# Optimization experiments

Measured on AMD Instinct MI355X. Metric: run time of the kernel, lower is better.

Reference implementation:

```python
import jax, jax.numpy as jnp
import numpy as np

C = 256
C8 = C // 8
B, H, W = 8, 64, 64


def setup_inputs() -> dict:
    key = jax.random.key(0)
    ks = jax.random.split(key, 8)
    scale = 1.0 / np.sqrt(C)
    return {
        "x": jax.random.normal(ks[0], (B, C, H, W), dtype=jnp.float32),
        "wq": jax.random.normal(ks[1], (C8, C), dtype=jnp.float32) * scale,
        "bq": jax.random.normal(ks[2], (C8,), dtype=jnp.float32) * 0.01,
        "wk": jax.random.normal(ks[3], (C8, C), dtype=jnp.float32) * scale,
        "bk": jax.random.normal(ks[4], (C8,), dtype=jnp.float32) * 0.01,
        "wv": jax.random.normal(ks[5], (C, C), dtype=jnp.float32) * scale,
        "bv": jax.random.normal(ks[6], (C,), dtype=jnp.float32) * 0.01,
        "gamma": jax.random.normal(ks[7], (1,), dtype=jnp.float32) * 0.1,
    }


def reference(x, wq, bq, wk, bk, wv, bv, gamma):
    b, c, h, w = x.shape
    n = h * w
    xf = x.reshape(b, c, n)  # flatten spatial; 1x1 conv == channel matmul
    q = jnp.einsum('oc,bcn->bno', wq, xf) + bq            # [b, n, c/8]
    k = jnp.einsum('oc,bcn->bon', wk, xf) + bk[:, None]   # [b, c/8, n]
    v = jnp.einsum('oc,bcn->bon', wv, xf) + bv[:, None]   # [b, c, n]
    attn = jax.nn.softmax(jnp.einsum('bno,bom->bnm', q, k), axis=2)  # [b,n,n]
    out = jnp.einsum('bcm,bnm->bcn', v, attn).reshape(b, c, h, w)
    return x + gamma[0] * out
```

## Files before the change

### kernel.cpp

```cpp
#include <hip/hip_runtime.h>

typedef unsigned short ushort_t;
typedef __bf16 bf16x8 __attribute__((ext_vector_type(8)));
typedef float f32x16 __attribute__((ext_vector_type(16)));
typedef float f32x4v __attribute__((ext_vector_type(4)));
typedef unsigned int u32x4 __attribute__((ext_vector_type(4)));
typedef unsigned int u32x2 __attribute__((ext_vector_type(2)));

#define L2E 1.44269504088896340736f

__device__ __forceinline__ unsigned cvt_pk_bf16(float a, float b) {
  unsigned r;
  asm("v_cvt_pk_bf16_f32 %0, %1, %2" : "=v"(r) : "v"(a), "v"(b));
  return r;
}

__device__ __forceinline__ float fast_exp2(float v) {
#if __has_builtin(__builtin_amdgcn_exp2f)
  return __builtin_amdgcn_exp2f(v);
#else
  return exp2f(v);
#endif
}

__device__ __forceinline__ f32x16 mfma32(u32x4 a, u32x4 b, f32x16 c) {
  return __builtin_amdgcn_mfma_f32_32x32x16_bf16(
      __builtin_bit_cast(bf16x8, a), __builtin_bit_cast(bf16x8, b), c, 0, 0, 0);
}

__global__ __launch_bounds__(512, 2) void proj_kernel(
    const float* __restrict__ x,
    const float* __restrict__ wq, const float* __restrict__ bq,
    const float* __restrict__ wk, const float* __restrict__ bk,
    const float* __restrict__ wv, const float* __restrict__ bv,
    ushort_t* __restrict__ qtg, ushort_t* __restrict__ ktg,
    ushort_t* __restrict__ vtg)
{
  __shared__ ushort_t xT[64 * 256];

  const int tid  = threadIdx.x;
  const int b    = blockIdx.x & 7;
  const int nt   = blockIdx.x >> 3;
  const int n0   = nt * 64;
  const int lane = tid & 63;
  const int wid  = tid >> 6;
  const int l31  = lane & 31;
  const int half = lane >> 5;

  {
    const int xn = tid & 63;
    const int cg = tid >> 6;
    const int ng = xn >> 5, l = xn & 31;
    const float* xb = x + (size_t)b * 256 * 4096 + n0 + xn;
    #pragma unroll
    for (int s = 0; s < 4; ++s) {
      const int c0 = cg * 32 + s * 8;
      float f0 = xb[(size_t)(c0+0)*4096], f1 = xb[(size_t)(c0+1)*4096];
      float f2 = xb[(size_t)(c0+2)*4096], f3 = xb[(size_t)(c0+3)*4096];
      float f4 = xb[(size_t)(c0+4)*4096], f5 = xb[(size_t)(c0+5)*4096];
      float f6 = xb[(size_t)(c0+6)*4096], f7 = xb[(size_t)(c0+7)*4096];
      u32x4 pk;
      pk.x = cvt_pk_bf16(f0, f1); pk.y = cvt_pk_bf16(f2, f3);
      pk.z = cvt_pk_bf16(f4, f5); pk.w = cvt_pk_bf16(f6, f7);
      const int c8 = c0 >> 3;
      *(u32x4*)(xT + ((c8 * 2 + ng) * 32 + l) * 8) = pk;
    }
  }
  __syncthreads();

  const int og = wid & 1, ng = (wid >> 1) & 1, rr = wid >> 2;
  const int n  = n0 + ng * 32 + l31;

  for (int ot = rr; ot < 5; ot += 2) {
    const int o0 = og * 160 + ot * 32;
    const int grow = o0 + l31;
    const float* wrow = (o0 < 32) ? (wq + grow * 256)
                      : (o0 < 64) ? (wk + (grow - 32) * 256)
                                  : (wv + (grow - 64) * 256);
    f32x16 acc = {};
    #pragma unroll
    for (int kc = 0; kc < 16; ++kc) {
      f32x4v g0 = *(const f32x4v*)(wrow + kc * 16 + half * 8);
      f32x4v g1 = *(const f32x4v*)(wrow + kc * 16 + half * 8 + 4);
      u32x4 af;
      af.x = cvt_pk_bf16(g0.x, g0.y); af.y = cvt_pk_bf16(g0.z, g0.w);
      af.z = cvt_pk_bf16(g1.x, g1.y); af.w = cvt_pk_bf16(g1.z, g1.w);
      u32x4 bf = *(const u32x4*)(xT + ((kc * 2 + half) * 2 + ng) * 256 + l31 * 8);
      acc = mfma32(af, bf, acc);
    }
    if (o0 < 64) {
      ushort_t* dst = (o0 == 0) ? qtg : ktg;
      const float* bias = (o0 == 0) ? bq : bk;
      const size_t rowbase = ((size_t)b * 4096 + n) * 32;
      #pragma unroll
      for (int g = 0; g < 4; ++g) {
        const int ob = 8 * g + 4 * half;
        float v0 = acc[4*g+0] + bias[ob+0];
        float v1 = acc[4*g+1] + bias[ob+1];
        float v2 = acc[4*g+2] + bias[ob+2];
        float v3 = acc[4*g+3] + bias[ob+3];
        u32x2 pk2; pk2.x = cvt_pk_bf16(v0, v1); pk2.y = cvt_pk_bf16(v2, v3);
        *(u32x2*)(dst + rowbase + ob) = pk2;
      }
    } else {
      const int cbase = o0 - 64;
      #pragma unroll
      for (int r = 0; r < 16; ++r) {
        const int c = cbase + (r & 3) + 8 * (r >> 2) + 4 * half;
        float v = acc[r] + bv[c];
        vtg[((size_t)b * 256 + c) * 4096 + n] = (ushort_t)cvt_pk_bf16(v, v);
      }
    }
  }
}

#define SOFTMAX_PACK(S, MR, LR, OB, PB0, PB1) do {                            \
  float y0 = fmaxf(fmaxf(S[0],  S[1]),  fmaxf(S[2],  S[3]));                  \
  float y1 = fmaxf(fmaxf(S[4],  S[5]),  fmaxf(S[6],  S[7]));                  \
  float y2 = fmaxf(fmaxf(S[8],  S[9]),  fmaxf(S[10], S[11]));                 \
  float y3 = fmaxf(fmaxf(S[12], S[13]), fmaxf(S[14], S[15]));                 \
  const float vmx  = fmaxf(fmaxf(y0, y1), fmaxf(y2, y3));                     \
  const float pmax = fmaxf(vmx, __shfl_xor(vmx, 32, 64));                     \
  if (__any(pmax > (MR) + 8.0f)) {                                            \
    const float mnew = fmaxf((MR), pmax);                                     \
    const float sc   = fast_exp2(((MR) - mnew) * L2E);                        \
    (LR) *= sc;                                                               \
    _Pragma("unroll")                                                         \
    for (int ct_ = 0; ct_ < 4; ++ct_) {                                       \
      _Pragma("unroll")                                                       \
      for (int r_ = 0; r_ < 16; ++r_) oacc[(OB) + ct_][r_] *= sc;             \
    }                                                                         \
    (MR) = mnew;                                                              \
  }                                                                           \
  const float ml2 = (MR) * L2E;                                               \
  float p_[16];                                                               \
  _Pragma("unroll")                                                           \
  for (int r_ = 0; r_ < 16; ++r_) p_[r_] = fast_exp2(fmaf(S[r_], L2E, -ml2)); \
  const float ps = (((p_[0]+p_[1])+(p_[2]+p_[3])) + ((p_[4]+p_[5])+(p_[6]+p_[7]))) \
                 + (((p_[8]+p_[9])+(p_[10]+p_[11])) + ((p_[12]+p_[13])+(p_[14]+p_[15]))); \
  (LR) += ps + __shfl_xor(ps, 32, 64);                                        \
  const unsigned wd0 = cvt_pk_bf16(p_[0],  p_[1]),  wd1 = cvt_pk_bf16(p_[2],  p_[3]);  \
  const unsigned wd2 = cvt_pk_bf16(p_[4],  p_[5]),  wd3 = cvt_pk_bf16(p_[6],  p_[7]);  \
  const unsigned wd4 = cvt_pk_bf16(p_[8],  p_[9]),  wd5 = cvt_pk_bf16(p_[10], p_[11]); \
  const unsigned wd6 = cvt_pk_bf16(p_[12], p_[13]), wd7 = cvt_pk_bf16(p_[14], p_[15]); \
  const unsigned pw0 = __shfl_xor((int)wd0, 32, 64), pw1 = __shfl_xor((int)wd1, 32, 64); \
  const unsigned pw2 = __shfl_xor((int)wd2, 32, 64), pw3 = __shfl_xor((int)wd3, 32, 64); \
  const unsigned pw4 = __shfl_xor((int)wd4, 32, 64), pw5 = __shfl_xor((int)wd5, 32, 64); \
  const unsigned pw6 = __shfl_xor((int)wd6, 32, 64), pw7 = __shfl_xor((int)wd7, 32, 64); \
  PB0.x = half ? pw2 : wd0;  PB0.y = half ? pw3 : wd1;                        \
  PB0.z = half ? wd2 : pw0;  PB0.w = half ? wd3 : pw1;                        \
  PB1.x = half ? pw6 : wd4;  PB1.y = half ? pw7 : wd5;                        \
  PB1.z = half ? wd6 : pw4;  PB1.w = half ? wd7 : pw5;                        \
} while (0)

__global__ __launch_bounds__(256, 2) void attn_kernel(
    const ushort_t* __restrict__ qtg, const ushort_t* __restrict__ ktg,
    const ushort_t* __restrict__ vtg, const float* __restrict__ x,
    const float* __restrict__ gamma, float* __restrict__ out)
{
  __shared__ float obuf[16][16][64];
  __shared__ float mls[2][8][64];

  const int tid  = threadIdx.x;
  const int lane = tid & 63;
  const int wid  = tid >> 6;
  const int l31  = lane & 31;
  const int half = lane >> 5;
  const int ks   = wid & 1;
  const int cs   = wid >> 1;
  const int b    = blockIdx.x & 7;
  const int qt   = blockIdx.x >> 3;
  const int qbase = qt * 64;

  const ushort_t* ktb = ktg + (size_t)b * 4096 * 32;
  const ushort_t* vr  = vtg + ((size_t)b * 256 + cs * 128 + l31) * 4096;

  const ushort_t* qr0 = qtg + ((size_t)b * 4096 + qbase + l31) * 32;
  const ushort_t* qr1 = qr0 + 32 * 32;
  const u32x4 qf00 = *(const u32x4*)(qr0 + half * 8);
  const u32x4 qf01 = *(const u32x4*)(qr0 + 16 + half * 8);
  const u32x4 qf10 = *(const u32x4*)(qr1 + half * 8);
  const u32x4 qf11 = *(const u32x4*)(qr1 + 16 + half * 8);

  u32x4 kf0 = *(const u32x4*)(ktb + (size_t)(ks * 32 + l31) * 32 + half * 8);
  u32x4 kf1 = *(const u32x4*)(ktb + (size_t)(ks * 32 + l31) * 32 + 16 + half * 8);
  u32x4 kn0 = kf0, kn1 = kf1;

  float mr0 = -3.0e38f, mr1 = -3.0e38f, lr0 = 0.0f, lr1 = 0.0f;
  f32x16 oacc[8] = {};

  for (int i = 0; i < 64; ++i) {
    const int t = 2 * i + ks;

    u32x4 vf[4][2];
    #pragma unroll
    for (int ct = 0; ct < 4; ++ct)
      #pragma unroll
      for (int mh = 0; mh < 2; ++mh)
        vf[ct][mh] = *(const u32x4*)(vr + (size_t)ct * 32 * 4096 +
                                     t * 32 + mh * 16 + half * 8);

    f32x16 s0 = {}, s1 = {};
    __builtin_amdgcn_s_setprio(1);
    s0 = mfma32(kf0, qf00, s0);  s0 = mfma32(kf1, qf01, s0);
    s1 = mfma32(kf0, qf10, s1);  s1 = mfma32(kf1, qf11, s1);
    __builtin_amdgcn_s_setprio(0);

    if (i < 63) {
      const ushort_t* kr = ktb + (size_t)((t + 2) * 32 + l31) * 32;
      kn0 = *(const u32x4*)(kr + half * 8);
      kn1 = *(const u32x4*)(kr + 16 + half * 8);
    }

    {
      u32x4 pb0, pb1;
      SOFTMAX_PACK(s0, mr0, lr0, 0, pb0, pb1);
      __builtin_amdgcn_s_setprio(1);
      #pragma unroll
      for (int ct = 0; ct < 4; ++ct) {
        oacc[ct] = mfma32(vf[ct][0], pb0, oacc[ct]);
        oacc[ct] = mfma32(vf[ct][1], pb1, oacc[ct]);
      }
      __builtin_amdgcn_s_setprio(0);
    }
    {
      u32x4 pb0, pb1;
      SOFTMAX_PACK(s1, mr1, lr1, 4, pb0, pb1);
      __builtin_amdgcn_s_setprio(1);
      #pragma unroll
      for (int ct = 0; ct < 4; ++ct) {
        oacc[4 + ct] = mfma32(vf[ct][0], pb0, oacc[4 + ct]);
        oacc[4 + ct] = mfma32(vf[ct][1], pb1, oacc[4 + ct]);
      }
      __builtin_amdgcn_s_setprio(0);
    }

    kf0 = kn0; kf1 = kn1;
  }

  mls[0][wid * 2 + 0][lane] = mr0;  mls[0][wid * 2 + 1][lane] = mr1;
  mls[1][wid * 2 + 0][lane] = lr0;  mls[1][wid * 2 + 1][lane] = lr1;
  __syncthreads();
  const int pw = (wid ^ 1) * 2;
  const float mO0 = mls[0][pw + 0][lane], lO0 = mls[1][pw + 0][lane];
  const float mO1 = mls[0][pw + 1][lane], lO1 = mls[1][pw + 1][lane];
  const float mS0 = fmaxf(mr0, mO0), mS1 = fmaxf(mr1, mO1);
  const float aS0 = fast_exp2((mr0 - mS0) * L2E), aO0 = fast_exp2((mO0 - mS0) * L2E);
  const float aS1 = fast_exp2((mr1 - mS1) * L2E), aO1 = fast_exp2((mO1 - mS1) * L2E);
  const float li0 = 1.0f / (aS0 * lr0 + aO0 * lO0);
  const float li1 = 1.0f / (aS1 * lr1 + aO1 * lO1);

  if (ks == 1) {
    #pragma unroll
    for (int qt2 = 0; qt2 < 2; ++qt2) {
      const float aS = qt2 ? aS1 : aS0;
      #pragma unroll
      for (int ct = 0; ct < 4; ++ct) {
        const int slot = cs * 8 + qt2 * 4 + ct;
        #pragma unroll
        for (int r = 0; r < 16; ++r)
          obuf[slot][r][lane] = aS * oacc[qt2 * 4 + ct][r];
      }
    }
  }
  __syncthreads();
  if (ks == 0) {
    const float g = gamma[0];
    const size_t base = (size_t)b * 256 * 4096;
    #pragma unroll
    for (int qt2 = 0; qt2 < 2; ++qt2) {
      const float aS = qt2 ? aS1 : aS0;
      const float li = qt2 ? li1 : li0;
      const size_t n = qbase + qt2 * 32 + l31;
      #pragma unroll
      for (int ct = 0; ct < 4; ++ct) {
        const int slot = cs * 8 + qt2 * 4 + ct;
        #pragma unroll
        for (int r = 0; r < 16; ++r) {
          const float oS = aS * oacc[qt2 * 4 + ct][r] + obuf[slot][r][lane];
          const int c = cs * 128 + ct * 32 + (r & 3) + 8 * (r >> 2) + 4 * half;
          const size_t off = base + (size_t)c * 4096 + n;
          out[off] = x[off] + g * (oS * li);
        }
      }
    }
  }
}

extern "C" void kernel_launch(void* const* d_in, const int* in_sizes, int n_in,
                              void* d_out, int out_size, void* d_ws, size_t ws_size,
                              hipStream_t stream) {
  (void)in_sizes; (void)n_in; (void)out_size; (void)ws_size;
  const float* x     = (const float*)d_in[0];
  const float* wq    = (const float*)d_in[1];
  const float* bq    = (const float*)d_in[2];
  const float* wk    = (const float*)d_in[3];
  const float* bk    = (const float*)d_in[4];
  const float* wv    = (const float*)d_in[5];
  const float* bv    = (const float*)d_in[6];
  const float* gamma = (const float*)d_in[7];
  float* out = (float*)d_out;

  ushort_t* ws  = (ushort_t*)d_ws;
  ushort_t* qtw = ws;
  ushort_t* ktw = ws + (size_t)8*4096*32;
  ushort_t* vww = ws + (size_t)2*8*4096*32;

  proj_kernel<<<512, 512, 0, stream>>>(x, wq, bq, wk, bk, wv, bv, qtw, ktw, vww);
  attn_kernel<<<512, 256, 0, stream>>>(qtw, ktw, vww, x, gamma, out);
}
```

Baseline: 285.4 us.

## Stage V tiles through LDS with async double buffering and stage projection weights

In the attention kernel, V tiles are no longer loaded from global memory straight into registers. Each wave now issues global_load_lds copies into a per-wave double-buffered LDS region one iteration ahead, synchronised with an explicit vmcnt wait, so the load latency can overlap with compute. The LDS is shared through a union with the output reduction buffer. The projection kernel also converts weights to bf16 into a swizzled LDS tile cooperatively and lets each wave compute two output tiles, which removes redundant per-wave global weight loads. The cost is more LDS use, which may lower occupancy, and hand-tuned waitcnt counts that are fragile.

```diff
diff --git a/kernel.cpp b/kernel.cpp
--- a/kernel.cpp
+++ b/kernel.cpp
@@ -37,6 +37,7 @@
     ushort_t* __restrict__ vtg)
 {
   __shared__ ushort_t xT[64 * 256];
+  __shared__ ushort_t wl[160 * 128];
 
   const int tid  = threadIdx.x;
   const int b    = blockIdx.x & 7;
@@ -63,52 +64,81 @@
       pk.x = cvt_pk_bf16(f0, f1); pk.y = cvt_pk_bf16(f2, f3);
       pk.z = cvt_pk_bf16(f4, f5); pk.w = cvt_pk_bf16(f6, f7);
       const int c8 = c0 >> 3;
-      *(u32x4*)(xT + ((c8 * 2 + ng) * 32 + l) * 8) = pk;
-    }
-  }
-  __syncthreads();
-
-  const int og = wid & 1, ng = (wid >> 1) & 1, rr = wid >> 2;
-  const int n  = n0 + ng * 32 + l31;
-
-  for (int ot = rr; ot < 5; ot += 2) {
-    const int o0 = og * 160 + ot * 32;
-    const int grow = o0 + l31;
-    const float* wrow = (o0 < 32) ? (wq + grow * 256)
-                      : (o0 < 64) ? (wk + (grow - 32) * 256)
-                                  : (wv + (grow - 64) * 256);
-    f32x16 acc = {};
-    #pragma unroll
-    for (int kc = 0; kc < 16; ++kc) {
-      f32x4v g0 = *(const f32x4v*)(wrow + kc * 16 + half * 8);
-      f32x4v g1 = *(const f32x4v*)(wrow + kc * 16 + half * 8 + 4);
-      u32x4 af;
-      af.x = cvt_pk_bf16(g0.x, g0.y); af.y = cvt_pk_bf16(g0.z, g0.w);
-      af.z = cvt_pk_bf16(g1.x, g1.y); af.w = cvt_pk_bf16(g1.z, g1.w);
-      u32x4 bf = *(const u32x4*)(xT + ((kc * 2 + half) * 2 + ng) * 256 + l31 * 8);
-      acc = mfma32(af, bf, acc);
-    }
-    if (o0 < 64) {
-      ushort_t* dst = (o0 == 0) ? qtg : ktg;
-      const float* bias = (o0 == 0) ? bq : bk;
-      const size_t rowbase = ((size_t)b * 4096 + n) * 32;
-      #pragma unroll
-      for (int g = 0; g < 4; ++g) {
-        const int ob = 8 * g + 4 * half;
-        float v0 = acc[4*g+0] + bias[ob+0];
-        float v1 = acc[4*g+1] + bias[ob+1];
-        float v2 = acc[4*g+2] + bias[ob+2];
-        float v3 = acc[4*g+3] + bias[ob+3];
-        u32x2 pk2; pk2.x = cvt_pk_bf16(v0, v1); pk2.y = cvt_pk_bf16(v2, v3);
-        *(u32x2*)(dst + rowbase + ob) = pk2;
-      }
-    } else {
-      const int cbase = o0 - 64;
-      #pragma unroll
-      for (int r = 0; r < 16; ++r) {
-        const int c = cbase + (r & 3) + 8 * (r >> 2) + 4 * half;
-        float v = acc[r] + bv[c];
-        vtg[((size_t)b * 256 + c) * 4096 + n] = (ushort_t)cvt_pk_bf16(v, v);
+      *(u32x4*)((char*)xT + (c8 * 2 + ng) * 512 + l * 16) = pk;
+    }
+  }
+
+  for (int h = 0; h < 2; ++h) {
+    f32x16 acc[2] = {};
+    #pragma unroll
+    for (int cc = 0; cc < 2; ++cc) {
+      __syncthreads();
+      #pragma unroll
+      for (int j = 0; j < 5; ++j) {
+        const int lin   = j * 512 + tid;
+        const int c8l   = lin & 15;
+        const int row_l = lin >> 4;
+        const int grow  = h * 160 + row_l;
+        const float* wrow = (grow < 32) ? (wq + grow * 256)
+                          : (grow < 64) ? (wk + (grow - 32) * 256)
+                                        : (wv + (grow - 64) * 256);
+        f32x4v g0 = *(const f32x4v*)(wrow + (cc * 16 + c8l) * 8);
+        f32x4v g1 = *(const f32x4v*)(wrow + (cc * 16 + c8l) * 8 + 4);
+        u32x4 pk;
+        pk.x = cvt_pk_bf16(g0.x, g0.y); pk.y = cvt_pk_bf16(g0.z, g0.w);
+        pk.z = cvt_pk_bf16(g1.x, g1.y); pk.w = cvt_pk_bf16(g1.z, g1.w);
+        const int addr = ((((row_l >> 5) * 8 + (c8l >> 1)) * 2 + (c8l & 1)) * 512
+                          + (row_l & 31) * 16) ^ ((c8l & 7) << 4);
+        *(u32x4*)((char*)wl + addr) = pk;
+      }
+      __syncthreads();
+      #pragma unroll
+      for (int tt = 0; tt < 2; ++tt) {
+        const int t = wid + tt * 8;
+        if (t < 10) {
+          const int ot = t >> 1, ng = t & 1;
+          #pragma unroll
+          for (int kc = 0; kc < 8; ++kc) {
+            const int aaddr = ((((ot * 8 + kc) * 2 + half) * 512) + l31 * 16)
+                              ^ (((kc * 2 + half) & 7) << 4);
+            u32x4 af = *(const u32x4*)((const char*)wl + aaddr);
+            const int c8g = cc * 16 + kc * 2 + half;
+            u32x4 bf = *(const u32x4*)((const char*)xT + (c8g * 2 + ng) * 512 + l31 * 16);
+            acc[tt] = mfma32(af, bf, acc[tt]);
+          }
+        }
+      }
+    }
+    #pragma unroll
+    for (int tt = 0; tt < 2; ++tt) {
+      const int t = wid + tt * 8;
+      if (t < 10) {
+        const int ot = t >> 1, ng = t & 1;
+        const int o0 = h * 160 + ot * 32;
+        const int n  = n0 + ng * 32 + l31;
+        if (o0 < 64) {
+          ushort_t* dst = (o0 == 0) ? qtg : ktg;
+          const float* bias = (o0 == 0) ? bq : bk;
+          const size_t rowbase = ((size_t)b * 4096 + n) * 32;
+          #pragma unroll
+          for (int g = 0; g < 4; ++g) {
+            const int ob = 8 * g + 4 * half;
+            float v0 = acc[tt][4*g+0] + bias[ob+0];
+            float v1 = acc[tt][4*g+1] + bias[ob+1];
+            float v2 = acc[tt][4*g+2] + bias[ob+2];
+            float v3 = acc[tt][4*g+3] + bias[ob+3];
+            u32x2 pk2; pk2.x = cvt_pk_bf16(v0, v1); pk2.y = cvt_pk_bf16(v2, v3);
+            *(u32x2*)(dst + rowbase + ob) = pk2;
+          }
+        } else {
+          const int cbase = o0 - 64;
+          #pragma unroll
+          for (int r = 0; r < 16; ++r) {
+            const int c = cbase + (r & 3) + 8 * (r >> 2) + 4 * half;
+            float v = acc[tt][r] + bv[c];
+            vtg[((size_t)b * 256 + c) * 4096 + n] = (ushort_t)cvt_pk_bf16(v, v);
+          }
+        }
       }
     }
   }
@@ -158,8 +188,7 @@
     const ushort_t* __restrict__ vtg, const float* __restrict__ x,
     const float* __restrict__ gamma, float* __restrict__ out)
 {
-  __shared__ float obuf[16][16][64];
-  __shared__ float mls[2][8][64];
+  __shared__ __align__(16) char smem[69632];
 
   const int tid  = threadIdx.x;
   const int lane = tid & 63;
@@ -173,7 +202,8 @@
   const int qbase = qt * 64;
 
   const ushort_t* ktb = ktg + (size_t)b * 4096 * 32;
-  const ushort_t* vr  = vtg + ((size_t)b * 256 + cs * 128 + l31) * 4096;
+  const ushort_t* vgb = vtg + (size_t)b * 256 * 4096;
+  char* vbuf = smem + wid * 16384;
 
   const ushort_t* qr0 = qtg + ((size_t)b * 4096 + qbase + l31) * 32;
   const ushort_t* qr1 = qr0 + 32 * 32;
@@ -182,23 +212,44 @@
   const u32x4 qf10 = *(const u32x4*)(qr1 + half * 8);
   const u32x4 qf11 = *(const u32x4*)(qr1 + 16 + half * 8);
 
+  #define STAGE_V(db, t_) do {                                                \
+    _Pragma("unroll")                                                         \
+    for (int j = 0; j < 8; ++j) {                                             \
+      const ushort_t* gp = vgb + (size_t)(cs*128 + (j>>1)*32 + l31)*4096      \
+                               + (t_)*32 + ((j&1)*2 + half)*8;                \
+      const char* lp = vbuf + (db)*8192 + j*1024;                             \
+      __builtin_amdgcn_global_load_lds(                                       \
+          (const __attribute__((address_space(1))) void*)gp,                  \
+          (__attribute__((address_space(3))) void*)lp, 16, 0, 0);             \
+    }                                                                         \
+  } while (0)
+
   u32x4 kf0 = *(const u32x4*)(ktb + (size_t)(ks * 32 + l31) * 32 + half * 8);
   u32x4 kf1 = *(const u32x4*)(ktb + (size_t)(ks * 32 + l31) * 32 + 16 + half * 8);
-  u32x4 kn0 = kf0, kn1 = kf1;
+  STAGE_V(0, ks);
 
   float mr0 = -3.0e38f, mr1 = -3.0e38f, lr0 = 0.0f, lr1 = 0.0f;
   f32x16 oacc[8] = {};
 
   for (int i = 0; i < 64; ++i) {
-    const int t = 2 * i + ks;
-
+    const int t  = 2 * i + ks;
+    const int tn = (i < 63) ? (t + 2) : t;
+
+    const ushort_t* kr = ktb + (size_t)(tn * 32 + l31) * 32;
+    u32x4 kn0 = *(const u32x4*)(kr + half * 8);
+    u32x4 kn1 = *(const u32x4*)(kr + 16 + half * 8);
+    STAGE_V((i + 1) & 1, tn);
+
+    asm volatile("s_waitcnt vmcnt(10)" ::: "memory");
+    __builtin_amdgcn_sched_barrier(0);
+
+    const char* vb = vbuf + (i & 1) * 8192;
     u32x4 vf[4][2];
     #pragma unroll
     for (int ct = 0; ct < 4; ++ct)
       #pragma unroll
       for (int mh = 0; mh < 2; ++mh)
-        vf[ct][mh] = *(const u32x4*)(vr + (size_t)ct * 32 * 4096 +
-                                     t * 32 + mh * 16 + half * 8);
+        vf[ct][mh] = *(const u32x4*)(vb + (ct*4 + mh*2 + half) * 512 + l31 * 16);
 
     f32x16 s0 = {}, s1 = {};
     __builtin_amdgcn_s_setprio(1);
@@ -206,12 +257,6 @@
     s1 = mfma32(kf0, qf10, s1);  s1 = mfma32(kf1, qf11, s1);
     __builtin_amdgcn_s_setprio(0);
 
-    if (i < 63) {
-      const ushort_t* kr = ktb + (size_t)((t + 2) * 32 + l31) * 32;
-      kn0 = *(const u32x4*)(kr + half * 8);
-      kn1 = *(const u32x4*)(kr + 16 + half * 8);
-    }
-
     {
       u32x4 pb0, pb1;
       SOFTMAX_PACK(s0, mr0, lr0, 0, pb0, pb1);
@@ -238,17 +283,24 @@
     kf0 = kn0; kf1 = kn1;
   }
 
-  mls[0][wid * 2 + 0][lane] = mr0;  mls[0][wid * 2 + 1][lane] = mr1;
-  mls[1][wid * 2 + 0][lane] = lr0;  mls[1][wid * 2 + 1][lane] = lr1;
+  asm volatile("s_waitcnt vmcnt(0)" ::: "memory");
+
+  float* mls = (float*)(smem + 65536);
+  mls[(0*8 + wid*2 + 0)*64 + lane] = mr0;
+  mls[(0*8 + wid*2 + 1)*64 + lane] = mr1;
+  mls[(1*8 + wid*2 + 0)*64 + lane] = lr0;
+  mls[(1*8 + wid*2 + 1)*64 + lane] = lr1;
   __syncthreads();
   const int pw = (wid ^ 1) * 2;
-  const float mO0 = mls[0][pw + 0][lane], lO0 = mls[1][pw + 0][lane];
-  const float mO1 = mls[0][pw + 1][lane], lO1 = mls[1][pw + 1][lane];
+  const float mO0 = mls[(0*8 + pw + 0)*64 + lane], lO0 = mls[(1*8 + pw + 0)*64 + lane];
+  const float mO1 = mls[(0*8 + pw + 1)*64 + lane], lO1 = mls[(1*8 + pw + 1)*64 + lane];
   const float mS0 = fmaxf(mr0, mO0), mS1 = fmaxf(mr1, mO1);
   const float aS0 = fast_exp2((mr0 - mS0) * L2E), aO0 = fast_exp2((mO0 - mS0) * L2E);
   const float aS1 = fast_exp2((mr1 - mS1) * L2E), aO1 = fast_exp2((mO1 - mS1) * L2E);
   const float li0 = 1.0f / (aS0 * lr0 + aO0 * lO0);
   const float li1 = 1.0f / (aS1 * lr1 + aO1 * lO1);
+
+  float (*obuf)[16][64] = (float (*)[16][64])smem;
 
   if (ks == 1) {
     #pragma unroll
```

Result: faster. 269.5 us (-5.6%).

## Tile V layout and stream V tiles into LDS with async double buffering

Applied to the files above, without the earlier changes.

The projection kernel now writes V in a tiled layout (per 32-key tile, contiguous 16 KB blocks), and the attention kernel prefetches each V tile into LDS with global_load_lds double buffering. This replaces strided per-lane global V loads. The projection kernel is also restructured: 10 waves each hold one output slice's weight fragments in registers, and two 32-column x tiles are staged one after the other. The changes bring more LDS usage (68 KB per block) and a manual vmcnt wait that relies on exact counts of outstanding loads.

```diff
diff --git a/kernel.cpp b/kernel.cpp
--- a/kernel.cpp
+++ b/kernel.cpp
@@ -28,7 +28,8 @@
       __builtin_bit_cast(bf16x8, a), __builtin_bit_cast(bf16x8, b), c, 0, 0, 0);
 }
 
-__global__ __launch_bounds__(512, 2) void proj_kernel(
+
+__global__ __launch_bounds__(640) void proj_kernel(
     const float* __restrict__ x,
     const float* __restrict__ wq, const float* __restrict__ bq,
     const float* __restrict__ wk, const float* __restrict__ bk,
@@ -36,82 +37,94 @@
     ushort_t* __restrict__ qtg, ushort_t* __restrict__ ktg,
     ushort_t* __restrict__ vtg)
 {
-  __shared__ ushort_t xT[64 * 256];
+  __shared__ ushort_t xT[2][32 * 256];
 
   const int tid  = threadIdx.x;
   const int b    = blockIdx.x & 7;
-  const int nt   = blockIdx.x >> 3;
-  const int n0   = nt * 64;
+  const int nb   = blockIdx.x >> 3;
+  const int tg0  = nb * 2;
   const int lane = tid & 63;
   const int wid  = tid >> 6;
   const int l31  = lane & 31;
   const int half = lane >> 5;
 
-  {
-    const int xn = tid & 63;
-    const int cg = tid >> 6;
-    const int ng = xn >> 5, l = xn & 31;
-    const float* xb = x + (size_t)b * 256 * 4096 + n0 + xn;
-    #pragma unroll
-    for (int s = 0; s < 4; ++s) {
-      const int c0 = cg * 32 + s * 8;
-      float f0 = xb[(size_t)(c0+0)*4096], f1 = xb[(size_t)(c0+1)*4096];
-      float f2 = xb[(size_t)(c0+2)*4096], f3 = xb[(size_t)(c0+3)*4096];
-      float f4 = xb[(size_t)(c0+4)*4096], f5 = xb[(size_t)(c0+5)*4096];
-      float f6 = xb[(size_t)(c0+6)*4096], f7 = xb[(size_t)(c0+7)*4096];
-      u32x4 pk;
-      pk.x = cvt_pk_bf16(f0, f1); pk.y = cvt_pk_bf16(f2, f3);
-      pk.z = cvt_pk_bf16(f4, f5); pk.w = cvt_pk_bf16(f6, f7);
-      const int c8 = c0 >> 3;
-      *(u32x4*)(xT + ((c8 * 2 + ng) * 32 + l) * 8) = pk;
-    }
+  const int o0 = wid * 32;
+  const int grow = o0 + l31;
+  const float* wrow = (o0 < 32) ? (wq + grow * 256)
+                    : (o0 < 64) ? (wk + (grow - 32) * 256)
+                                : (wv + (grow - 64) * 256);
+  u32x4 af[16];
+  #pragma unroll
+  for (int kc = 0; kc < 16; ++kc) {
+    f32x4v g0 = *(const f32x4v*)(wrow + kc * 16 + half * 8);
+    f32x4v g1 = *(const f32x4v*)(wrow + kc * 16 + half * 8 + 4);
+    af[kc].x = cvt_pk_bf16(g0.x, g0.y); af[kc].y = cvt_pk_bf16(g0.z, g0.w);
+    af[kc].z = cvt_pk_bf16(g1.x, g1.y); af[kc].w = cvt_pk_bf16(g1.z, g1.w);
   }
+
+  #define STAGE_X(db, tg) do {                                                \
+    if (wid < 8) {                                                            \
+      const int xn = tid & 31;                                                \
+      const int cg = tid >> 5;                                     \
+      const float* xb = x + (size_t)b * 256 * 4096 + (tg) * 32 + xn;          \
+      _Pragma("unroll")                                                       \
+      for (int s = 0; s < 2; ++s) {                                           \
+        const int c8 = cg * 2 + s;                                            \
+        const int c0 = c8 * 8;                                                \
+        float f0 = xb[(size_t)(c0+0)*4096], f1 = xb[(size_t)(c0+1)*4096];     \
+        float f2 = xb[(size_t)(c0+2)*4096], f3 = xb[(size_t)(c0+3)*4096];     \
+        float f4 = xb[(size_t)(c0+4)*4096], f5 = xb[(size_t)(c0+5)*4096];     \
+        float f6 = xb[(size_t)(c0+6)*4096], f7 = xb[(size_t)(c0+7)*4096];     \
+        u32x4 pk;                                                             \
+        pk.x = cvt_pk_bf16(f0, f1); pk.y = cvt_pk_bf16(f2, f3);               \
+        pk.z = cvt_pk_bf16(f4, f5); pk.w = cvt_pk_bf16(f6, f7);               \
+        *(u32x4*)((char*)xT[db] + c8 * 512 + xn * 16) = pk;                   \
+      }                                                                       \
+    }                                                                         \
+  } while (0)
+
+  #define COMPUTE_STORE(db, tg) do {                                          \
+    f32x16 acc = {};                                                          \
+    _Pragma("unroll")                                                         \
+    for (int kc = 0; kc < 16; ++kc) {                                         \
+      u32x4 bf = *(const u32x4*)((char*)xT[db] + (kc*2 + half) * 512 + l31 * 16); \
+      acc = mfma32(af[kc], bf, acc);                                          \
+    }                                                                         \
+    const int n = (tg) * 32 + l31;                                            \
+    if (o0 < 64) {                                                            \
+      ushort_t* dst = (o0 == 0) ? qtg : ktg;                                  \
+      const float* bias = (o0 == 0) ? bq : bk;                                \
+      const size_t rowbase = ((size_t)b * 4096 + n) * 32;                     \
+      _Pragma("unroll")                                                       \
+      for (int g = 0; g < 4; ++g) {                                           \
+        const int ob = 8 * g + 4 * half;                                      \
+        float v0 = acc[4*g+0] + bias[ob+0];                                   \
+        float v1 = acc[4*g+1] + bias[ob+1];                                   \
+        float v2 = acc[4*g+2] + bias[ob+2];                                   \
+        float v3 = acc[4*g+3] + bias[ob+3];                                   \
+        u32x2 pk2; pk2.x = cvt_pk_bf16(v0, v1); pk2.y = cvt_pk_bf16(v2, v3);  \
+        *(u32x2*)(dst + rowbase + ob) = pk2;                                  \
+      }                                                                       \
+    } else {                                                                  \
+      const int cbase = o0 - 64;                                              \
+      char* tb = (char*)vtg + (size_t)(b * 128 + (tg)) * 16384;               \
+      _Pragma("unroll")                                                       \
+      for (int r = 0; r < 16; ++r) {                                          \
+        const int c = cbase + (r & 3) + 8 * (r >> 2) + 4 * half;              \
+        const int m = l31;                                                    \
+        float v = acc[r] + bv[c];                                             \
+        *(ushort_t*)(tb + (((c >> 5) * 4 + (m >> 3)) * 32 + (c & 31)) * 16    \
+                        + (m & 7) * 2) = (ushort_t)cvt_pk_bf16(v, v);         \
+      }                                                                       \
+    }                                                                         \
+  } while (0)
+
+  STAGE_X(0, tg0);
   __syncthreads();
-
-  const int og = wid & 1, ng = (wid >> 1) & 1, rr = wid >> 2;
-  const int n  = n0 + ng * 32 + l31;
-
-  for (int ot = rr; ot < 5; ot += 2) {
-    const int o0 = og * 160 + ot * 32;
-    const int grow = o0 + l31;
-    const float* wrow = (o0 < 32) ? (wq + grow * 256)
-                      : (o0 < 64) ? (wk + (grow - 32) * 256)
-                                  : (wv + (grow - 64) * 256);
-    f32x16 acc = {};
-    #pragma unroll
-    for (int kc = 0; kc < 16; ++kc) {
-      f32x4v g0 = *(const f32x4v*)(wrow + kc * 16 + half * 8);
-      f32x4v g1 = *(const f32x4v*)(wrow + kc * 16 + half * 8 + 4);
-      u32x4 af;
-      af.x = cvt_pk_bf16(g0.x, g0.y); af.y = cvt_pk_bf16(g0.z, g0.w);
-      af.z = cvt_pk_bf16(g1.x, g1.y); af.w = cvt_pk_bf16(g1.z, g1.w);
-      u32x4 bf = *(const u32x4*)(xT + ((kc * 2 + half) * 2 + ng) * 256 + l31 * 8);
-      acc = mfma32(af, bf, acc);
-    }
-    if (o0 < 64) {
-      ushort_t* dst = (o0 == 0) ? qtg : ktg;
-      const float* bias = (o0 == 0) ? bq : bk;
-      const size_t rowbase = ((size_t)b * 4096 + n) * 32;
-      #pragma unroll
-      for (int g = 0; g < 4; ++g) {
-        const int ob = 8 * g + 4 * half;
-        float v0 = acc[4*g+0] + bias[ob+0];
-        float v1 = acc[4*g+1] + bias[ob+1];
-        float v2 = acc[4*g+2] + bias[ob+2];
-        float v3 = acc[4*g+3] + bias[ob+3];
-        u32x2 pk2; pk2.x = cvt_pk_bf16(v0, v1); pk2.y = cvt_pk_bf16(v2, v3);
-        *(u32x2*)(dst + rowbase + ob) = pk2;
-      }
-    } else {
-      const int cbase = o0 - 64;
-      #pragma unroll
-      for (int r = 0; r < 16; ++r) {
-        const int c = cbase + (r & 3) + 8 * (r >> 2) + 4 * half;
-        float v = acc[r] + bv[c];
-        vtg[((size_t)b * 256 + c) * 4096 + n] = (ushort_t)cvt_pk_bf16(v, v);
-      }
-    }
-  }
+  STAGE_X(1, tg0 + 1);
+  COMPUTE_STORE(0, tg0);
+  __syncthreads();
+  COMPUTE_STORE(1, tg0 + 1);
 }
 
 #define SOFTMAX_PACK(S, MR, LR, OB, PB0, PB1) do {                            \
@@ -158,8 +171,7 @@
     const ushort_t* __restrict__ vtg, const float* __restrict__ x,
     const float* __restrict__ gamma, float* __restrict__ out)
 {
-  __shared__ float obuf[16][16][64];
-  __shared__ float mls[2][8][64];
+  __shared__ __align__(16) char smem[69632];
 
   const int tid  = threadIdx.x;
   const int lane = tid & 63;
@@ -173,7 +185,7 @@
   const int qbase = qt * 64;
 
   const ushort_t* ktb = ktg + (size_t)b * 4096 * 32;
-  const ushort_t* vr  = vtg + ((size_t)b * 256 + cs * 128 + l31) * 4096;
+  char* vbuf = smem + wid * 16384;
 
   const ushort_t* qr0 = qtg + ((size_t)b * 4096 + qbase + l31) * 32;
   const ushort_t* qr1 = qr0 + 32 * 32;
@@ -182,35 +194,50 @@
   const u32x4 qf10 = *(const u32x4*)(qr1 + half * 8);
   const u32x4 qf11 = *(const u32x4*)(qr1 + 16 + half * 8);
 
+  #define STAGE_V(db, t_) do {                                                \
+    const char* tb = (const char*)vtg + (size_t)(b * 128 + (t_)) * 16384      \
+                     + cs * 8192 + lane * 16;                                 \
+    _Pragma("unroll")                                                         \
+    for (int j = 0; j < 8; ++j) {                                             \
+      __builtin_amdgcn_global_load_lds(                                       \
+          (const __attribute__((address_space(1))) void*)(tb + j * 1024),     \
+          (__attribute__((address_space(3))) void*)(vbuf + (db)*8192 + j*1024), \
+          16, 0, 0);                                                          \
+    }                                                                         \
+  } while (0)
+
   u32x4 kf0 = *(const u32x4*)(ktb + (size_t)(ks * 32 + l31) * 32 + half * 8);
   u32x4 kf1 = *(const u32x4*)(ktb + (size_t)(ks * 32 + l31) * 32 + 16 + half * 8);
-  u32x4 kn0 = kf0, kn1 = kf1;
+  STAGE_V(0, ks);
 
   float mr0 = -3.0e38f, mr1 = -3.0e38f, lr0 = 0.0f, lr1 = 0.0f;
   f32x16 oacc[8] = {};
 
   for (int i = 0; i < 64; ++i) {
-    const int t = 2 * i + ks;
-
+    const int t  = 2 * i + ks;
+    const int tn = (i < 63) ? (t + 2) : t;
+
+    const ushort_t* kr = ktb + (size_t)(tn * 32 + l31) * 32;
+    u32x4 kn0 = *(const u32x4*)(kr + half * 8);
+    u32x4 kn1 = *(const u32x4*)(kr + 16 + half * 8);
+    STAGE_V((i + 1) & 1, tn);
+
+    asm volatile("s_waitcnt vmcnt(10)" ::: "memory");
+    __builtin_amdgcn_sched_barrier(0);
+
+    const char* vb = vbuf + (i & 1) * 8192;
     u32x4 vf[4][2];
     #pragma unroll
     for (int ct = 0; ct < 4; ++ct)
       #pragma unroll
       for (int mh = 0; mh < 2; ++mh)
-        vf[ct][mh] = *(const u32x4*)(vr + (size_t)ct * 32 * 4096 +
-                                     t * 32 + mh * 16 + half * 8);
+        vf[ct][mh] = *(const u32x4*)(vb + (ct*4 + mh*2 + half) * 512 + l31 * 16);
 
     f32x16 s0 = {}, s1 = {};
     __builtin_amdgcn_s_setprio(1);
     s0 = mfma32(kf0, qf00, s0);  s0 = mfma32(kf1, qf01, s0);
     s1 = mfma32(kf0, qf10, s1);  s1 = mfma32(kf1, qf11, s1);
     __builtin_amdgcn_s_setprio(0);
-
-    if (i < 63) {
-      const ushort_t* kr = ktb + (size_t)((t + 2) * 32 + l31) * 32;
-      kn0 = *(const u32x4*)(kr + half * 8);
-      kn1 = *(const u32x4*)(kr + 16 + half * 8);
-    }
 
     {
       u32x4 pb0, pb1;
@@ -238,17 +265,24 @@
     kf0 = kn0; kf1 = kn1;
   }
 
-  mls[0][wid * 2 + 0][lane] = mr0;  mls[0][wid * 2 + 1][lane] = mr1;
-  mls[1][wid * 2 + 0][lane] = lr0;  mls[1][wid * 2 + 1][lane] = lr1;
+  asm volatile("s_waitcnt vmcnt(0)" ::: "memory");
+
+  float* mls = (float*)(smem + 65536);
+  mls[(0*8 + wid*2 + 0)*64 + lane] = mr0;
+  mls[(0*8 + wid*2 + 1)*64 + lane] = mr1;
+  mls[(1*8 + wid*2 + 0)*64 + lane] = lr0;
+  mls[(1*8 + wid*2 + 1)*64 + lane] = lr1;
   __syncthreads();
   const int pw = (wid ^ 1) * 2;
-  const float mO0 = mls[0][pw + 0][lane], lO0 = mls[1][pw + 0][lane];
-  const float mO1 = mls[0][pw + 1][lane], lO1 = mls[1][pw + 1][lane];
+  const float mO0 = mls[(0*8 + pw + 0)*64 + lane], lO0 = mls[(1*8 + pw + 0)*64 + lane];
+  const float mO1 = mls[(0*8 + pw + 1)*64 + lane], lO1 = mls[(1*8 + pw + 1)*64 + lane];
   const float mS0 = fmaxf(mr0, mO0), mS1 = fmaxf(mr1, mO1);
   const float aS0 = fast_exp2((mr0 - mS0) * L2E), aO0 = fast_exp2((mO0 - mS0) * L2E);
   const float aS1 = fast_exp2((mr1 - mS1) * L2E), aO1 = fast_exp2((mO1 - mS1) * L2E);
   const float li0 = 1.0f / (aS0 * lr0 + aO0 * lO0);
   const float li1 = 1.0f / (aS1 * lr1 + aO1 * lO1);
+
+  float (*obuf)[16][64] = (float (*)[16][64])smem;
 
   if (ks == 1) {
     #pragma unroll
@@ -306,6 +340,6 @@
   ushort_t* ktw = ws + (size_t)8*4096*32;
   ushort_t* vww = ws + (size_t)2*8*4096*32;
 
-  proj_kernel<<<512, 512, 0, stream>>>(x, wq, bq, wk, bk, wv, bv, qtw, ktw, vww);
+  proj_kernel<<<512, 640, 0, stream>>>(x, wq, bq, wk, bk, wv, bv, qtw, ktw, vww);
   attn_kernel<<<512, 256, 0, stream>>>(qtw, ktw, vww, x, gamma, out);
 }
```

Result: faster. 260.7 us (-8.7%).
